# Kernel optimization log

Hardware: AMD Instinct MI355X
Metric: run time of the kernel (lower is better)

The kernel has to match this reference:

```python
import jax, jax.numpy as jnp
import numpy as np

EPS = 1e-5

def bn_relu(x, g, b):
    # BatchNorm (training-mode batch stats, biased var) + ReLU.
    # x: (..., C); per-channel stats over all leading axes.
    axes = tuple(range(x.ndim - 1))
    m = jnp.mean(x, axes, keepdims=True)
    v = jnp.var(x, axes, keepdims=True)
    return jax.nn.relu((x - m) * jax.lax.rsqrt(v + EPS) * g + b)

def knn_idx(xyz, k):
    # xyz: (B,N,3) -> (B,N,k) indices of k nearest neighbors (incl. self)
    sq = jnp.sum(xyz * xyz, -1)
    d2 = sq[:, :, None] + sq[:, None, :] - 2.0 * jnp.einsum('bnd,bmd->bnm', xyz, xyz)
    return jax.lax.top_k(-d2, k)[1]

def group(xyz, feat, k):
    # PCT sample_and_group (no FPS): gather KNN feats, concat(rel, center)
    idx = knn_idx(xyz, k)                                        # (B,N,K)
    grouped = jnp.take_along_axis(feat[:, None, :, :], idx[..., None], axis=2)  # (B,N,K,d)
    center = feat[:, :, None, :]
    return jnp.concatenate([grouped - center, jnp.broadcast_to(center, grouped.shape)], -1)

def local_op(x, W1, g1, b1, W2, g2, b2):
    # x: (B,N,K,d_i). Torch reshapes to (B*N,d_i,K): BN stats over (B,N,K).
    h = bn_relu(jnp.einsum('bnkd,od->bnko', x, W1), g1, b1)
    h = bn_relu(jnp.einsum('bnkd,od->bnko', h, W2), g2, b2)
    return jnp.max(h, axis=2)                                    # adaptive_max_pool1d(.,1)

def setup_inputs() -> dict:
    key = jax.random.key(0)
    ks = jax.random.split(key, 8)
    B, N = 8, 1024
    d_i, d_h1, d_h2, d_h3, d_o = 3, 64, 256, 512, 1024
    s = 0.02
    inp = {
        'xyz': jax.random.normal(ks[0], (B, N, d_i), jnp.float32),
        'W1': jax.random.normal(ks[1], (d_h1, d_i), jnp.float32) * s,
        'g1': jnp.ones((d_h1,), jnp.float32), 'b1': jnp.zeros((d_h1,), jnp.float32),
        'W2': jax.random.normal(ks[2], (d_h2, d_h1), jnp.float32) * s,
        'g2': jnp.ones((d_h2,), jnp.float32), 'b2': jnp.zeros((d_h2,), jnp.float32),
        'WA1': jax.random.normal(ks[3], (d_h3, d_h3), jnp.float32) * s,
        'gA1': jnp.ones((d_h3,), jnp.float32), 'bA1': jnp.zeros((d_h3,), jnp.float32),
        'WA2': jax.random.normal(ks[4], (d_h3, d_h3), jnp.float32) * s,
        'gA2': jnp.ones((d_h3,), jnp.float32), 'bA2': jnp.zeros((d_h3,), jnp.float32),
        'WB1': jax.random.normal(ks[5], (d_o, d_o), jnp.float32) * s,
        'gB1': jnp.ones((d_o,), jnp.float32), 'bB1': jnp.zeros((d_o,), jnp.float32),
        'WB2': jax.random.normal(ks[6], (d_o, d_o), jnp.float32) * s,
        'gB2': jnp.ones((d_o,), jnp.float32), 'bB2': jnp.zeros((d_o,), jnp.float32),
        'n_sample': 8,
    }
    return inp

def reference(xyz, W1, g1, b1, W2, g2, b2, WA1, gA1, bA1, WA2, gA2, bA2,
              WB1, gB1, bB1, WB2, gB2, bB2, n_sample):
    # pointwise conv-bn-relu stack on raw points (channel-last)
    h = bn_relu(jnp.einsum('bni,oi->bno', xyz, W1), g1, b1)      # (B,N,64)
    h = bn_relu(jnp.einsum('bni,oi->bno', h, W2), g2, b2)        # (B,N,256)
    g0 = group(xyz, h, n_sample)                                  # (B,N,K,512)
    l0 = local_op(g0, WA1, gA1, bA1, WA2, gA2, bA2)              # (B,N,512)
    g1_ = group(xyz, l0, n_sample)                                # (B,N,K,1024)
    l1 = local_op(g1_, WB1, gB1, bB1, WB2, gB2, bB2)             # (B,N,1024)
    return jnp.transpose(l1, (0, 2, 1))                           # (B,1024,N)
```

## Files before the change

### kernel.cpp

```cpp
#include <hip/hip_runtime.h>
#include <stdint.h>

typedef __bf16 bf8_t __attribute__((ext_vector_type(8)));
typedef float f32x4 __attribute__((ext_vector_type(4)));

#define EPSV 1e-5f

__device__ __forceinline__ float b2f(unsigned short u) {
  union { uint32_t i; float f; } v; v.i = ((uint32_t)u) << 16; return v.f;
}
__device__ __forceinline__ unsigned short f2b(float f) {
  union { float f; uint32_t i; } v; v.f = f;
  uint32_t x = v.i;
  return (unsigned short)((x + 0x7fffu + ((x >> 16) & 1u)) >> 16);
}

typedef __attribute__((address_space(1))) void gvoid;
typedef __attribute__((address_space(3))) void lvoid;
__device__ __forceinline__ void gload16(const unsigned short* g, unsigned short* l) {
  __builtin_amdgcn_global_load_lds((gvoid*)g, (lvoid*)l, 16, 0, 0);
}

__global__ __launch_bounds__(256) void cvt_f2b(const float* __restrict__ in,
                                               unsigned short* __restrict__ out, int n) {
  int gid = blockIdx.x * 256 + threadIdx.x;
  if (gid < n) out[gid] = f2b(in[gid]);
}

__global__ __launch_bounds__(256) void stage1(const float* __restrict__ xyz,
                                              const float* __restrict__ W1,
                                              float* __restrict__ y1) {
  int gid = blockIdx.x * 256 + threadIdx.x;
  int r = gid >> 6, o = gid & 63;
  float x0 = xyz[r*3+0], x1 = xyz[r*3+1], x2 = xyz[r*3+2];
  float w0 = W1[o*3+0], w1 = W1[o*3+1], w2 = W1[o*3+2];
  y1[gid] = x0*w0 + x1*w1 + x2*w2;
}

__global__ __launch_bounds__(256) void colstats(const float* __restrict__ y, int O,
                                                float* __restrict__ acc) {
  int col = blockIdx.x * 64 + (threadIdx.x & 63);
  long rbase = (long)blockIdx.y * 1024 + (threadIdx.x >> 6);
  float s = 0.f, s2 = 0.f;
  for (int i = 0; i < 256; ++i) {
    float v = y[(rbase + (long)i*4) * O + col];
    s += v; s2 += v*v;
  }
  __shared__ float red[512];
  red[threadIdx.x] = s; red[256 + threadIdx.x] = s2;
  __syncthreads();
  if (threadIdx.x < 64) {
    float S = 0.f, S2 = 0.f;
    for (int j = 0; j < 4; ++j) { S += red[threadIdx.x + 64*j]; S2 += red[256 + threadIdx.x + 64*j]; }
    atomicAdd(&acc[col], S);
    atomicAdd(&acc[O + col], S2);
  }
}

__global__ void finalize_stats(const float* __restrict__ acc, const float* __restrict__ g,
                               const float* __restrict__ b, int O, float invCount,
                               float* __restrict__ a, float* __restrict__ cc) {
  int c = blockIdx.x * 256 + threadIdx.x;
  if (c >= O) return;
  float m = acc[c] * invCount;
  float v = fmaxf(acc[O + c] * invCount - m*m, 0.f);
  float rs = rsqrtf(v + EPSV);
  float A = g[c] * rs;
  a[c] = A; cc[c] = b[c] - m * A;
}

__global__ __launch_bounds__(256) void bnrelu_cast(const float* __restrict__ y,
                                                   const float* __restrict__ a,
                                                   const float* __restrict__ cc,
                                                   int Omask,
                                                   unsigned short* __restrict__ out) {
  long base = ((long)blockIdx.x * 256 + threadIdx.x) * 8;
  int c = (int)(base & (long)Omask);
  float4 f0 = *(const float4*)(y + base);
  float4 f1 = *(const float4*)(y + base + 4);
  float4 a0 = *(const float4*)(a + c);
  float4 a1 = *(const float4*)(a + c + 4);
  float4 c0 = *(const float4*)(cc + c);
  float4 c1 = *(const float4*)(cc + c + 4);
  uint4 v;
  unsigned short* u = (unsigned short*)&v;
  u[0] = f2b(fmaxf(a0.x*f0.x + c0.x, 0.f));
  u[1] = f2b(fmaxf(a0.y*f0.y + c0.y, 0.f));
  u[2] = f2b(fmaxf(a0.z*f0.z + c0.z, 0.f));
  u[3] = f2b(fmaxf(a0.w*f0.w + c0.w, 0.f));
  u[4] = f2b(fmaxf(a1.x*f1.x + c1.x, 0.f));
  u[5] = f2b(fmaxf(a1.y*f1.y + c1.y, 0.f));
  u[6] = f2b(fmaxf(a1.z*f1.z + c1.z, 0.f));
  u[7] = f2b(fmaxf(a1.w*f1.w + c1.w, 0.f));
  *(uint4*)(out + base) = v;
}

__global__ __launch_bounds__(256) void gstats(const float* __restrict__ Z,
                                              const float* __restrict__ C,
                                              const int* __restrict__ fs,
                                              int S, int O,
                                              float* __restrict__ acc) {
  const int t = threadIdx.x;
  const int cq = O >> 2;
  const int c = (t & (cq - 1)) << 2;
  const int rof = t / cq;
  const int rstep = 256 / cq;
  const long rbase = (long)blockIdx.x * 128;
  float s0=0,s1=0,s2=0,s3=0, q0=0,q1=0,q2=0,q3=0;
  for (int r = rof; r < 128; r += rstep) {
    const long rr = rbase + r;
    const long zr = (long)fs[rr] * S;
    const long cr = (rr >> 3) * (long)S;
    float4 z = *(const float4*)(Z + zr + c);
    float4 y = *(const float4*)(C + cr + c);
    float v0=z.x+y.x, v1=z.y+y.y, v2=z.z+y.z, v3=z.w+y.w;
    s0+=v0; s1+=v1; s2+=v2; s3+=v3;
    q0+=v0*v0; q1+=v1*v1; q2+=v2*v2; q3+=v3*v3;
  }
  atomicAdd(&acc[c+0], s0); atomicAdd(&acc[c+1], s1);
  atomicAdd(&acc[c+2], s2); atomicAdd(&acc[c+3], s3);
  atomicAdd(&acc[O+c+0], q0); atomicAdd(&acc[O+c+1], q1);
  atomicAdd(&acc[O+c+2], q2); atomicAdd(&acc[O+c+3], q3);
}

__global__ __launch_bounds__(256) void gbn(const float* __restrict__ Z,
                                           const float* __restrict__ C,
                                           const int* __restrict__ fs,
                                           const float* __restrict__ a,
                                           const float* __restrict__ cc,
                                           int S,
                                           int cprShift,
                                           unsigned short* __restrict__ out) {
  const int O = 8 << cprShift;
  long gid = (long)blockIdx.x * 256 + threadIdx.x;
  long r = gid >> cprShift;
  int c = (int)(gid & ((1 << cprShift) - 1)) << 3;
  const long zr = (long)fs[r] * S;
  const long cr = (r >> 3) * (long)S;
  float4 z0 = *(const float4*)(Z + zr + c), z1 = *(const float4*)(Z + zr + c + 4);
  float4 y0 = *(const float4*)(C + cr + c), y1 = *(const float4*)(C + cr + c + 4);
  float4 a0 = *(const float4*)(a + c),      a1 = *(const float4*)(a + c + 4);
  float4 b0 = *(const float4*)(cc + c),     b1 = *(const float4*)(cc + c + 4);
  uint4 v; unsigned short* u = (unsigned short*)&v;
  u[0] = f2b(fmaxf(a0.x*(z0.x+y0.x) + b0.x, 0.f));
  u[1] = f2b(fmaxf(a0.y*(z0.y+y0.y) + b0.y, 0.f));
  u[2] = f2b(fmaxf(a0.z*(z0.z+y0.z) + b0.z, 0.f));
  u[3] = f2b(fmaxf(a0.w*(z0.w+y0.w) + b0.w, 0.f));
  u[4] = f2b(fmaxf(a1.x*(z1.x+y1.x) + b1.x, 0.f));
  u[5] = f2b(fmaxf(a1.y*(z1.y+y1.y) + b1.y, 0.f));
  u[6] = f2b(fmaxf(a1.z*(z1.z+y1.z) + b1.z, 0.f));
  u[7] = f2b(fmaxf(a1.w*(z1.w+y1.w) + b1.w, 0.f));
  *(uint4*)(out + r*O + c) = v;
}

__global__ __launch_bounds__(256) void knn_kernel(const float* __restrict__ xyz,
                                                  int* __restrict__ flat_src) {
  __shared__ float px[1024], py[1024], pz[1024], sq[1024];
  int b = blockIdx.x;
  for (int i = threadIdx.x; i < 1024; i += 256) {
    float x = xyz[(b*1024 + i)*3 + 0];
    float y = xyz[(b*1024 + i)*3 + 1];
    float z = xyz[(b*1024 + i)*3 + 2];
    px[i] = x; py[i] = y; pz[i] = z; sq[i] = x*x + y*y + z*z;
  }
  __syncthreads();
  int q = blockIdx.y * 256 + threadIdx.x;
  float qx = px[q], qy = py[q], qz = pz[q], qs = sq[q];
  float bd[8]; int bi[8];
  #pragma unroll
  for (int j = 0; j < 8; ++j) { bd[j] = 3.4e38f; bi[j] = 0; }
  for (int m = 0; m < 1024; ++m) {
    float dot = qx*px[m] + qy*py[m] + qz*pz[m];
    float d2 = qs + sq[m] - 2.f*dot;
    if (d2 < bd[7]) {
      bd[7] = d2; bi[7] = m;
      #pragma unroll
      for (int j = 7; j > 0; --j) {
        if (bd[j] < bd[j-1]) {
          float td = bd[j]; bd[j] = bd[j-1]; bd[j-1] = td;
          int ti = bi[j]; bi[j] = bi[j-1]; bi[j-1] = ti;
        }
      }
    }
  }
  #pragma unroll
  for (int j = 0; j < 8; ++j) flat_src[(b*1024 + q)*8 + j] = b*1024 + bi[j];
}

__global__ __launch_bounds__(256) void wdiff(const float* __restrict__ W, int H,
                                             unsigned short* __restrict__ WD) {
  int gid = blockIdx.x * 256 + threadIdx.x;
  int o = gid / H, h = gid - o*H;
  WD[gid] = f2b(W[o*2*H + H + h] - W[o*2*H + h]);
}

__global__ __launch_bounds__(256) void cvt_lo(const float* __restrict__ W, int H,
                                              unsigned short* __restrict__ out) {
  int gid = blockIdx.x * 256 + threadIdx.x;
  int o = gid / H, h = gid - o*H;
  out[gid] = f2b(W[o*2*H + h]);
}

union GemmSmem {
  struct { unsigned short A[128*64]; unsigned short W[128*64]; } st;
  struct { float redS[128*8]; float redS2[128*8]; } fst;
};

__global__ __launch_bounds__(256) void gemm_kernel(
    const unsigned short* __restrict__ A16,
    long strideA,
    const int* __restrict__ rowmap,
    const unsigned short* __restrict__ W, int strideW,
    int K, int O,
    const float* __restrict__ addC,
    unsigned short* __restrict__ outB,
    float* __restrict__ outF,
    float* __restrict__ statsP,
    float* __restrict__ ymax, float* __restrict__ ymin,
    float* __restrict__ statsMM)
{
  __shared__ GemmSmem sm;

  const int t = threadIdx.x;
  const int wave = t >> 6, lane = t & 63, quad = lane >> 4, lr = lane & 15;
  const int wr0 = (wave >> 1) * 64, wc0 = (wave & 1) * 64;

  const int nwgx = gridDim.x;
  const int nwg = nwgx * gridDim.y;
  const int id = blockIdx.y * nwgx + blockIdx.x;
  const int swz = (id & 7) * (nwg >> 3) + (id >> 3);
  const int rowB = swz / nwgx;
  const int colB = swz - rowB * nwgx;
  const long rowBase = (long)rowB * 128;
  const int colBase = colB * 128;

  const int lrow = lane >> 3;
  const int lchk = ((lane & 7) ^ lrow) << 3;
  const unsigned short* pa[4];
  const unsigned short* pw[4];
  #pragma unroll
  for (int j = 0; j < 4; ++j) {
    int r = wave*32 + j*8 + lrow;
    long sA = rowmap ? (long)rowmap[rowBase + r] : rowBase + r;
    pa[j] = A16 + sA * strideA + lchk;
    pw[j] = W + (long)(colBase + r) * strideW + lchk;
  }

  f32x4 acc[4][4];
  #pragma unroll
  for (int i = 0; i < 4; ++i)
    #pragma unroll
    for (int j = 0; j < 4; ++j)
      acc[i][j] = (f32x4){0.f, 0.f, 0.f, 0.f};

  for (int k0 = 0; k0 < K; k0 += 64) {
    __syncthreads();
    #pragma unroll
    for (int j = 0; j < 4; ++j) {
      gload16(pa[j] + k0, &sm.st.A[wave*2048 + j*512]);
      gload16(pw[j] + k0, &sm.st.W[wave*2048 + j*512]);
    }
    __syncthreads();

    #pragma unroll
    for (int kk = 0; kk < 2; ++kk) {
      const int coff = (((kk*4 + quad) ^ (lr & 7)) << 3);
      bf8_t af[4], bfr[4];
      #pragma unroll
      for (int s = 0; s < 4; ++s) {
        af[s]  = *(const bf8_t*)&sm.st.A[(wr0 + s*16 + lr)*64 + coff];
        bfr[s] = *(const bf8_t*)&sm.st.W[(wc0 + s*16 + lr)*64 + coff];
      }
      #pragma unroll
      for (int sr = 0; sr < 4; ++sr)
        #pragma unroll
        for (int sc = 0; sc < 4; ++sc)
          acc[sr][sc] = __builtin_amdgcn_mfma_f32_16x16x32_bf16(af[sr], bfr[sc], acc[sr][sc], 0, 0, 0);
    }
  }

  if (!ymax) {
    float s[4] = {0.f,0.f,0.f,0.f}, s2[4] = {0.f,0.f,0.f,0.f};
    #pragma unroll
    for (int sc = 0; sc < 4; ++sc) {
      int col = colBase + wc0 + sc*16 + lr;
      #pragma unroll
      for (int sr = 0; sr < 4; ++sr) {
        #pragma unroll
        for (int r = 0; r < 4; ++r) {
          long row = rowBase + wr0 + sr*16 + quad*4 + r;
          float v = acc[sr][sc][r];
          if (addC) v += addC[(row >> 3) * (long)O + col];
          if (outF) outF[row * (long)O + col] = v;
          else      outB[row * (long)O + col] = f2b(v);
          s[sc] += v; s2[sc] += v*v;
        }
      }
    }
    if (statsP) {
      __syncthreads();
      int q8 = quad + 4*(wave >> 1);
      #pragma unroll
      for (int sc = 0; sc < 4; ++sc) {
        int colL = wc0 + sc*16 + lr;
        sm.fst.redS[colL*8 + q8]  = s[sc];
        sm.fst.redS2[colL*8 + q8] = s2[sc];
      }
      __syncthreads();
      if (t < 128) {
        float S = 0.f, S2 = 0.f;
        #pragma unroll
        for (int j = 0; j < 8; ++j) { S += sm.fst.redS[t*8 + j]; S2 += sm.fst.redS2[t*8 + j]; }
        atomicAdd(&statsP[colBase + t], S);
        atomicAdd(&statsP[O + colBase + t], S2);
      }
    }
  } else {
    #pragma unroll
    for (int sc = 0; sc < 4; ++sc) {
      int col = colBase + wc0 + sc*16 + lr;
      float s = 0.f, s2v = 0.f;
      #pragma unroll
      for (int sr = 0; sr < 4; ++sr) {
        float mx = acc[sr][sc][0], mn = acc[sr][sc][0];
        s += acc[sr][sc][0]; s2v += acc[sr][sc][0]*acc[sr][sc][0];
        #pragma unroll
        for (int r = 1; r < 4; ++r) {
          float v = acc[sr][sc][r];
          mx = fmaxf(mx, v); mn = fminf(mn, v);
          s += v; s2v += v*v;
        }
        mx = fmaxf(mx, __shfl_xor(mx, 16));
        mn = fminf(mn, __shfl_xor(mn, 16));
        if ((quad & 1) == 0) {
          long orow = (long)rowB*16 + (wave >> 1)*8 + sr*2 + (quad >> 1);
          ymax[orow * O + col] = mx;
          ymin[orow * O + col] = mn;
        }
      }
      s   += __shfl_xor(s, 16);   s   += __shfl_xor(s, 32);
      s2v += __shfl_xor(s2v, 16); s2v += __shfl_xor(s2v, 32);
      if (quad == 0) {
        atomicAdd(&statsMM[col], s);
        atomicAdd(&statsMM[O + col], s2v);
      }
    }
  }
}

__global__ __launch_bounds__(256) void to_l0(const float* __restrict__ ymax,
                                             const float* __restrict__ ymin,
                                             const float* __restrict__ a, const float* __restrict__ cc,
                                             unsigned short* __restrict__ l0) {
  int gid = blockIdx.x * 256 + threadIdx.x;
  int c = gid & 511;
  float A = a[c];
  float v = (A >= 0.f) ? ymax[gid] : ymin[gid];
  l0[gid] = f2b(fmaxf(A*v + cc[c], 0.f));
}

__global__ __launch_bounds__(256) void final_out(const float* __restrict__ ymax,
                                                 const float* __restrict__ ymin,
                                                 const float* __restrict__ a, const float* __restrict__ cc,
                                                 float* __restrict__ out) {
  __shared__ float tile[32][33];
  int b = blockIdx.x, ct = blockIdx.y * 32, nt = blockIdx.z * 32;
  int tc = threadIdx.x & 31, tr = threadIdx.x >> 5;
  #pragma unroll
  for (int i = 0; i < 4; ++i) {
    int n = nt + tr + i*8;
    int c = ct + tc;
    float A = a[c];
    long idx = ((long)(b*1024 + n))*1024 + c;
    float v = (A >= 0.f) ? ymax[idx] : ymin[idx];
    tile[tr + i*8][tc] = fmaxf(A*v + cc[c], 0.f);
  }
  __syncthreads();
  #pragma unroll
  for (int i = 0; i < 4; ++i) {
    int c = ct + tr + i*8;
    int n = nt + tc;
    out[((long)(b*1024 + c))*1024 + n] = tile[tc][tr + i*8];
  }
}

extern "C" void kernel_launch(void* const* d_in, const int* in_sizes, int n_in,
                              void* d_out, int out_size, void* d_ws, size_t ws_size,
                              hipStream_t stream) {
  const float* xyz = (const float*)d_in[0];
  const float* W1  = (const float*)d_in[1];
  const float* g1  = (const float*)d_in[2];
  const float* b1  = (const float*)d_in[3];
  const float* W2  = (const float*)d_in[4];
  const float* g2  = (const float*)d_in[5];
  const float* b2  = (const float*)d_in[6];
  const float* WA1 = (const float*)d_in[7];
  const float* gA1 = (const float*)d_in[8];
  const float* bA1 = (const float*)d_in[9];
  const float* WA2 = (const float*)d_in[10];
  const float* gA2 = (const float*)d_in[11];
  const float* bA2 = (const float*)d_in[12];
  const float* WB1 = (const float*)d_in[13];
  const float* gB1 = (const float*)d_in[14];
  const float* bB1 = (const float*)d_in[15];
  const float* WB2 = (const float*)d_in[16];
  const float* gB2 = (const float*)d_in[17];
  const float* bB2 = (const float*)d_in[18];
  float* out = (float*)d_out;

  char* w = (char*)d_ws;
  const size_t MB = 1048576;

  size_t off = 0;
  auto nxt = [&](size_t bytes) { void* p = w + off; off = (off + bytes + 255) & ~(size_t)255; return p; };
  int*            flat_src = (int*)nxt(262144);
  unsigned short* W2b   = (unsigned short*)nxt(32768);
  unsigned short* WcatA = (unsigned short*)nxt(524288);
  unsigned short* WA2b  = (unsigned short*)nxt(524288);
  unsigned short* WcatB = (unsigned short*)nxt(2097152);
  unsigned short* WB2b  = (unsigned short*)nxt(2097152);
  float* statsZone = (float*)nxt(27136);
  float* affZone   = (float*)nxt(27136);

  float*          y1f   = (float*)(w + 193*MB);
  unsigned short* x2in  = (unsigned short*)(w + 195*MB);
  float*          y2f   = (float*)(w + 196*MB);
  unsigned short* xA1   = (unsigned short*)(w + 204*MB);
  float*          YA    = (float*)(w + 8*MB);
  unsigned short* xA2   = (unsigned short*)(w + 40*MB);
  float*          ymaxA = (float*)(w + 104*MB);
  float*          yminA = (float*)(w + 120*MB);
  unsigned short* l0    = (unsigned short*)(w + 136*MB);
  float*          YB    = (float*)(w + 8*MB);
  unsigned short* yB1b  = (unsigned short*)(w + 72*MB);
  float*          ymaxB = (float*)(w + 8*MB);
  float*          yminB = (float*)(w + 40*MB);

  float* acc1  = statsZone;
  float* acc2  = statsZone + 128;
  float* accA1 = statsZone + 640;
  float* accA2 = statsZone + 1664;
  float* accB1 = statsZone + 2688;
  float* accB2 = statsZone + 4736;

  float* a1  = affZone;        float* cc1  = affZone + 64;
  float* a2  = affZone + 128;  float* cc2  = affZone + 384;
  float* aA1 = affZone + 640;  float* ccA1 = affZone + 1152;
  float* aA2 = affZone + 1664; float* ccA2 = affZone + 2176;
  float* aB1 = affZone + 2688; float* ccB1 = affZone + 3712;
  float* aB2 = affZone + 4736; float* ccB2 = affZone + 5760;

  hipMemsetAsync(statsZone, 0, 6784 * 4, stream);

  cvt_f2b<<<64, 256, 0, stream>>>(W2, W2b, 16384);
  wdiff<<<512, 256, 0, stream>>>(WA1, 256, WcatA);
  cvt_lo<<<512, 256, 0, stream>>>(WA1, 256, WcatA + 131072);
  cvt_f2b<<<1024, 256, 0, stream>>>(WA2, WA2b, 262144);
  wdiff<<<2048, 256, 0, stream>>>(WB1, 512, WcatB);
  cvt_lo<<<2048, 256, 0, stream>>>(WB1, 512, WcatB + 524288);
  cvt_f2b<<<4096, 256, 0, stream>>>(WB2, WB2b, 1048576);

  stage1<<<2048, 256, 0, stream>>>(xyz, W1, y1f);
  colstats<<<dim3(1, 8), 256, 0, stream>>>(y1f, 64, acc1);
  finalize_stats<<<1, 256, 0, stream>>>(acc1, g1, b1, 64, 1.f/8192.f, a1, cc1);
  bnrelu_cast<<<256, 256, 0, stream>>>(y1f, a1, cc1, 63, x2in);

  gemm_kernel<<<dim3(2, 64), 256, 0, stream>>>(x2in, 64, nullptr,
                                               W2b, 64, 64, 256,
                                               nullptr, nullptr, y2f, acc2, nullptr, nullptr, nullptr);
  finalize_stats<<<1, 256, 0, stream>>>(acc2, g2, b2, 256, 1.f/8192.f, a2, cc2);
  bnrelu_cast<<<1024, 256, 0, stream>>>(y2f, a2, cc2, 255, xA1);

  knn_kernel<<<dim3(8, 4), 256, 0, stream>>>(xyz, flat_src);

  gemm_kernel<<<dim3(8, 64), 256, 0, stream>>>(xA1, 256, nullptr,
                                               WcatA, 256, 256, 1024,
                                               nullptr, nullptr, YA, nullptr, nullptr, nullptr, nullptr);
  gstats<<<512, 256, 0, stream>>>(YA + 512, YA, flat_src, 1024, 512, accA1);
  finalize_stats<<<2, 256, 0, stream>>>(accA1, gA1, bA1, 512, 1.f/65536.f, aA1, ccA1);
  gbn<<<16384, 256, 0, stream>>>(YA + 512, YA, flat_src, aA1, ccA1, 1024, 6, xA2);

  gemm_kernel<<<dim3(4, 512), 256, 0, stream>>>(xA2, 512, nullptr,
                                                WA2b, 512, 512, 512,
                                                nullptr, nullptr, nullptr, nullptr, ymaxA, yminA, accA2);
  finalize_stats<<<2, 256, 0, stream>>>(accA2, gA2, bA2, 512, 1.f/65536.f, aA2, ccA2);
  to_l0<<<16384, 256, 0, stream>>>(ymaxA, yminA, aA2, ccA2, l0);

  gemm_kernel<<<dim3(16, 64), 256, 0, stream>>>(l0, 512, nullptr,
                                                WcatB, 512, 512, 2048,
                                                nullptr, nullptr, YB, nullptr, nullptr, nullptr, nullptr);
  gstats<<<512, 256, 0, stream>>>(YB + 1024, YB, flat_src, 2048, 1024, accB1);
  finalize_stats<<<4, 256, 0, stream>>>(accB1, gB1, bB1, 1024, 1.f/65536.f, aB1, ccB1);
  gbn<<<32768, 256, 0, stream>>>(YB + 1024, YB, flat_src, aB1, ccB1, 2048, 7, yB1b);

  gemm_kernel<<<dim3(8, 512), 256, 0, stream>>>(yB1b, 1024, nullptr,
                                                WB2b, 1024, 1024, 1024,
                                                nullptr, nullptr, nullptr, nullptr, ymaxB, yminB, accB2);
  finalize_stats<<<4, 256, 0, stream>>>(accB2, gB2, bB2, 1024, 1.f/65536.f, aB2, ccB2);

  final_out<<<dim3(8, 32, 32), 256, 0, stream>>>(ymaxB, yminB, aB2, ccB2, out);
}
```

Baseline: 1.105 ms.

## Double-buffer GEMM LDS tiles to overlap global loads with MFMA compute

Splits the shared-memory A/W tiles into two buffers and issues the next k-tile's global-to-LDS loads before computing on the current tile, with one wait and barrier per iteration instead of two syncthreads. The aim is to hide global load latency behind the MFMA work. It doubles LDS use per block to 64KB, which can lower occupancy. It also relies on inline waitcnt and barrier for correctness, with no explicit wait for LDS reads to finish before the buffer is overwritten.

```diff
diff --git a/kernel.cpp b/kernel.cpp
--- a/kernel.cpp
+++ b/kernel.cpp
@@ -202,7 +202,7 @@
 }
 
 union GemmSmem {
-  struct { unsigned short A[128*64]; unsigned short W[128*64]; } st;
+  struct { unsigned short A[2][8192]; unsigned short W[2][8192]; } st;
   struct { float redS[128*8]; float redS2[128*8]; } fst;
 };
 
@@ -253,14 +253,27 @@
     for (int j = 0; j < 4; ++j)
       acc[i][j] = (f32x4){0.f, 0.f, 0.f, 0.f};
 
-  for (int k0 = 0; k0 < K; k0 += 64) {
-    __syncthreads();
-    #pragma unroll
-    for (int j = 0; j < 4; ++j) {
-      gload16(pa[j] + k0, &sm.st.A[wave*2048 + j*512]);
-      gload16(pw[j] + k0, &sm.st.W[wave*2048 + j*512]);
+  const int nt = K >> 6;
+
+  #pragma unroll
+  for (int j = 0; j < 4; ++j) {
+    gload16(pa[j], &sm.st.A[0][wave*2048 + j*512]);
+    gload16(pw[j], &sm.st.W[0][wave*2048 + j*512]);
+  }
+  asm volatile("s_waitcnt vmcnt(0)" ::: "memory");
+  __builtin_amdgcn_s_barrier();
+
+  int cur = 0;
+  for (int tt = 0; tt < nt; ++tt) {
+    if (tt + 1 < nt) {
+      const long koff = (long)(tt + 1) << 6;
+      #pragma unroll
+      for (int j = 0; j < 4; ++j) {
+        gload16(pa[j] + koff, &sm.st.A[cur ^ 1][wave*2048 + j*512]);
+        gload16(pw[j] + koff, &sm.st.W[cur ^ 1][wave*2048 + j*512]);
+      }
     }
-    __syncthreads();
+    asm volatile("" ::: "memory");
 
     #pragma unroll
     for (int kk = 0; kk < 2; ++kk) {
@@ -268,8 +281,8 @@
       bf8_t af[4], bfr[4];
       #pragma unroll
       for (int s = 0; s < 4; ++s) {
-        af[s]  = *(const bf8_t*)&sm.st.A[(wr0 + s*16 + lr)*64 + coff];
-        bfr[s] = *(const bf8_t*)&sm.st.W[(wc0 + s*16 + lr)*64 + coff];
+        af[s]  = *(const bf8_t*)&sm.st.A[cur][(wr0 + s*16 + lr)*64 + coff];
+        bfr[s] = *(const bf8_t*)&sm.st.W[cur][(wc0 + s*16 + lr)*64 + coff];
       }
       #pragma unroll
       for (int sr = 0; sr < 4; ++sr)
@@ -277,6 +290,10 @@
         for (int sc = 0; sc < 4; ++sc)
           acc[sr][sc] = __builtin_amdgcn_mfma_f32_16x16x32_bf16(af[sr], bfr[sc], acc[sr][sc], 0, 0, 0);
     }
+
+    asm volatile("s_waitcnt vmcnt(0)" ::: "memory");
+    __builtin_amdgcn_s_barrier();
+    cur ^= 1;
   }
 
   if (!ymax) {
```

New measurement: 1.108 ms. Within noise of the previous version (+0.3%).

## Load GEMM MFMA operands directly from global into registers, drop LDS staging

Applied to the files above, without the earlier changes.

Replaces the global_load_lds staging of A and W tiles into shared memory with direct per-lane 16-byte global loads into registers that feed the MFMA instructions. This removes the two block barriers per k-step and the LDS reads. In exchange, the two waves sharing each tile row or column load it redundantly, which doubles global/L2 traffic. Load latency is also exposed directly before the MFMAs. The unused rowmap parameter is dropped and the shared buffer is shrunk to the stats reduction area.

```diff
diff --git a/kernel.cpp b/kernel.cpp
--- a/kernel.cpp
+++ b/kernel.cpp
@@ -13,12 +13,6 @@
   union { float f; uint32_t i; } v; v.f = f;
   uint32_t x = v.i;
   return (unsigned short)((x + 0x7fffu + ((x >> 16) & 1u)) >> 16);
-}
-
-typedef __attribute__((address_space(1))) void gvoid;
-typedef __attribute__((address_space(3))) void lvoid;
-__device__ __forceinline__ void gload16(const unsigned short* g, unsigned short* l) {
-  __builtin_amdgcn_global_load_lds((gvoid*)g, (lvoid*)l, 16, 0, 0);
 }
 
 __global__ __launch_bounds__(256) void cvt_f2b(const float* __restrict__ in,
@@ -201,15 +195,9 @@
   out[gid] = f2b(W[o*2*H + h]);
 }
 
-union GemmSmem {
-  struct { unsigned short A[128*64]; unsigned short W[128*64]; } st;
-  struct { float redS[128*8]; float redS2[128*8]; } fst;
-};
-
 __global__ __launch_bounds__(256) void gemm_kernel(
     const unsigned short* __restrict__ A16,
     long strideA,
-    const int* __restrict__ rowmap,
     const unsigned short* __restrict__ W, int strideW,
     int K, int O,
     const float* __restrict__ addC,
@@ -219,7 +207,7 @@
     float* __restrict__ ymax, float* __restrict__ ymin,
     float* __restrict__ statsMM)
 {
-  __shared__ GemmSmem sm;
+  __shared__ float red[2048];
 
   const int t = threadIdx.x;
   const int wave = t >> 6, lane = t & 63, quad = lane >> 4, lr = lane & 15;
@@ -234,16 +222,12 @@
   const long rowBase = (long)rowB * 128;
   const int colBase = colB * 128;
 
-  const int lrow = lane >> 3;
-  const int lchk = ((lane & 7) ^ lrow) << 3;
   const unsigned short* pa[4];
   const unsigned short* pw[4];
   #pragma unroll
-  for (int j = 0; j < 4; ++j) {
-    int r = wave*32 + j*8 + lrow;
-    long sA = rowmap ? (long)rowmap[rowBase + r] : rowBase + r;
-    pa[j] = A16 + sA * strideA + lchk;
-    pw[j] = W + (long)(colBase + r) * strideW + lchk;
+  for (int s = 0; s < 4; ++s) {
+    pa[s] = A16 + (rowBase + wr0 + s*16 + lr) * strideA + quad*8;
+    pw[s] = W + (long)(colBase + wc0 + s*16 + lr) * strideW + quad*8;
   }
 
   f32x4 acc[4][4];
@@ -254,29 +238,22 @@
       acc[i][j] = (f32x4){0.f, 0.f, 0.f, 0.f};
 
   for (int k0 = 0; k0 < K; k0 += 64) {
-    __syncthreads();
+    uint4 va[4][2], vw[4][2];
     #pragma unroll
-    for (int j = 0; j < 4; ++j) {
-      gload16(pa[j] + k0, &sm.st.A[wave*2048 + j*512]);
-      gload16(pw[j] + k0, &sm.st.W[wave*2048 + j*512]);
+    for (int s = 0; s < 4; ++s) {
+      va[s][0] = *(const uint4*)(pa[s] + k0);
+      va[s][1] = *(const uint4*)(pa[s] + k0 + 32);
+      vw[s][0] = *(const uint4*)(pw[s] + k0);
+      vw[s][1] = *(const uint4*)(pw[s] + k0 + 32);
     }
-    __syncthreads();
-
     #pragma unroll
-    for (int kk = 0; kk < 2; ++kk) {
-      const int coff = (((kk*4 + quad) ^ (lr & 7)) << 3);
-      bf8_t af[4], bfr[4];
-      #pragma unroll
-      for (int s = 0; s < 4; ++s) {
-        af[s]  = *(const bf8_t*)&sm.st.A[(wr0 + s*16 + lr)*64 + coff];
-        bfr[s] = *(const bf8_t*)&sm.st.W[(wc0 + s*16 + lr)*64 + coff];
-      }
+    for (int kk = 0; kk < 2; ++kk)
       #pragma unroll
       for (int sr = 0; sr < 4; ++sr)
         #pragma unroll
         for (int sc = 0; sc < 4; ++sc)
-          acc[sr][sc] = __builtin_amdgcn_mfma_f32_16x16x32_bf16(af[sr], bfr[sc], acc[sr][sc], 0, 0, 0);
-    }
+          acc[sr][sc] = __builtin_amdgcn_mfma_f32_16x16x32_bf16(
+              *(const bf8_t*)&va[sr][kk], *(const bf8_t*)&vw[sc][kk], acc[sr][sc], 0, 0, 0);
   }
 
   if (!ymax) {
@@ -298,19 +275,18 @@
       }
     }
     if (statsP) {
-      __syncthreads();
       int q8 = quad + 4*(wave >> 1);
       #pragma unroll
       for (int sc = 0; sc < 4; ++sc) {
         int colL = wc0 + sc*16 + lr;
-        sm.fst.redS[colL*8 + q8]  = s[sc];
-        sm.fst.redS2[colL*8 + q8] = s2[sc];
+        red[colL*8 + q8]          = s[sc];
+        red[1024 + colL*8 + q8]   = s2[sc];
       }
       __syncthreads();
       if (t < 128) {
         float S = 0.f, S2 = 0.f;
         #pragma unroll
-        for (int j = 0; j < 8; ++j) { S += sm.fst.redS[t*8 + j]; S2 += sm.fst.redS2[t*8 + j]; }
+        for (int j = 0; j < 8; ++j) { S += red[t*8 + j]; S2 += red[1024 + t*8 + j]; }
         atomicAdd(&statsP[colBase + t], S);
         atomicAdd(&statsP[O + colBase + t], S2);
       }
@@ -465,7 +441,7 @@
   finalize_stats<<<1, 256, 0, stream>>>(acc1, g1, b1, 64, 1.f/8192.f, a1, cc1);
   bnrelu_cast<<<256, 256, 0, stream>>>(y1f, a1, cc1, 63, x2in);
 
-  gemm_kernel<<<dim3(2, 64), 256, 0, stream>>>(x2in, 64, nullptr,
+  gemm_kernel<<<dim3(2, 64), 256, 0, stream>>>(x2in, 64,
                                                W2b, 64, 64, 256,
                                                nullptr, nullptr, y2f, acc2, nullptr, nullptr, nullptr);
   finalize_stats<<<1, 256, 0, stream>>>(acc2, g2, b2, 256, 1.f/8192.f, a2, cc2);
@@ -473,27 +449,27 @@
 
   knn_kernel<<<dim3(8, 4), 256, 0, stream>>>(xyz, flat_src);
 
-  gemm_kernel<<<dim3(8, 64), 256, 0, stream>>>(xA1, 256, nullptr,
+  gemm_kernel<<<dim3(8, 64), 256, 0, stream>>>(xA1, 256,
                                                WcatA, 256, 256, 1024,
                                                nullptr, nullptr, YA, nullptr, nullptr, nullptr, nullptr);
   gstats<<<512, 256, 0, stream>>>(YA + 512, YA, flat_src, 1024, 512, accA1);
   finalize_stats<<<2, 256, 0, stream>>>(accA1, gA1, bA1, 512, 1.f/65536.f, aA1, ccA1);
   gbn<<<16384, 256, 0, stream>>>(YA + 512, YA, flat_src, aA1, ccA1, 1024, 6, xA2);
 
-  gemm_kernel<<<dim3(4, 512), 256, 0, stream>>>(xA2, 512, nullptr,
+  gemm_kernel<<<dim3(4, 512), 256, 0, stream>>>(xA2, 512,
                                                 WA2b, 512, 512, 512,
                                                 nullptr, nullptr, nullptr, nullptr, ymaxA, yminA, accA2);
   finalize_stats<<<2, 256, 0, stream>>>(accA2, gA2, bA2, 512, 1.f/65536.f, aA2, ccA2);
   to_l0<<<16384, 256, 0, stream>>>(ymaxA, yminA, aA2, ccA2, l0);
 
-  gemm_kernel<<<dim3(16, 64), 256, 0, stream>>>(l0, 512, nullptr,
+  gemm_kernel<<<dim3(16, 64), 256, 0, stream>>>(l0, 512,
                                                 WcatB, 512, 512, 2048,
                                                 nullptr, nullptr, YB, nullptr, nullptr, nullptr, nullptr);
   gstats<<<512, 256, 0, stream>>>(YB + 1024, YB, flat_src, 2048, 1024, accB1);
   finalize_stats<<<4, 256, 0, stream>>>(accB1, gB1, bB1, 1024, 1.f/65536.f, aB1, ccB1);
   gbn<<<32768, 256, 0, stream>>>(YB + 1024, YB, flat_src, aB1, ccB1, 2048, 7, yB1b);
 
-  gemm_kernel<<<dim3(8, 512), 256, 0, stream>>>(yB1b, 1024, nullptr,
+  gemm_kernel<<<dim3(8, 512), 256, 0, stream>>>(yB1b, 1024,
                                                 WB2b, 1024, 1024, 1024,
                                                 nullptr, nullptr, nullptr, nullptr, ymaxB, yminB, accB2);
   finalize_stats<<<4, 256, 0, stream>>>(accB2, gB2, bB2, 1024, 1.f/65536.f, aB2, ccB2);
```

Measured after the change: 1.362 ms. +23.2%, slower.
